# Kernel tuning notes

Hardware: AMD Instinct MI355X
Metric: run time of the kernel (lower is better)

## Reference

```python
import jax, jax.numpy as jnp
import numpy as np

# Coefficients expressing each of the 16 soft binary logic gates as
# c0 + ca*a + cb*b + cab*(a*b), in standard difflogic op order:
# 0:False 1:AND 2:a&~b 3:A 4:~a&b 5:B 6:XOR 7:OR 8:NOR 9:XNOR
# 10:~B 11:B=>A 12:~A 13:A=>B 14:NAND 15:True
GATE_COEF = jnp.array([
    [0, 0, 0, 0],
    [0, 0, 0, 1],
    [0, 1, 0, -1],
    [0, 1, 0, 0],
    [0, 0, 1, -1],
    [0, 0, 1, 0],
    [0, 1, 1, -2],
    [0, 1, 1, -1],
    [1, -1, -1, 1],
    [1, -1, -1, 2],
    [1, 0, -1, 0],
    [1, 0, -1, 1],
    [1, -1, 0, 0],
    [1, -1, 0, 1],
    [1, 0, 0, -1],
    [1, 0, 0, 0],
], dtype=jnp.float32)  # [16, 4]

INPUT_DIM = 8192
HIDDEN_DIMS = [16384, 16384, 16384, 16384]
OUTPUT_DIM = 1000
BATCH = 2048
TAU = 1.0
N_GATES = 16


def setup_inputs() -> dict:
    key = jax.random.key(0)
    kx, key = jax.random.split(key)
    inp = {"x": jax.random.uniform(kx, (BATCH, INPUT_DIM), dtype=jnp.float32)}
    dims = [INPUT_DIM] + HIDDEN_DIMS + [OUTPUT_DIM]
    for i in range(len(dims) - 1):
        in_d, out_d = dims[i], dims[i + 1]
        kw, ka, kb, key = jax.random.split(key, 4)
        inp[f"w{i}"] = jax.random.normal(kw, (out_d, N_GATES), dtype=jnp.float32)
        inp[f"ia{i}"] = jax.random.randint(ka, (out_d,), 0, in_d, dtype=jnp.int32)
        inp[f"ib{i}"] = jax.random.randint(kb, (out_d,), 0, in_d, dtype=jnp.int32)
    return inp


def _logic_layer(x, w, ia, ib):
    # gather the two inputs of every neuron: [batch, out_dim]
    a = x[:, ia]
    b = x[:, ib]
    p = jax.nn.softmax(w, axis=-1)              # [out_dim, 16]
    coef = p @ GATE_COEF                         # [out_dim, 4]
    # weighted mixture of all 16 gates, fused via bilinear form
    return coef[:, 0] + coef[:, 1] * a + coef[:, 2] * b + coef[:, 3] * (a * b)


def reference(x, w0, w1, w2, w3, w4, ia0, ia1, ia2, ia3, ia4, ib0, ib1, ib2, ib3, ib4):
    ws = [w0, w1, w2, w3, w4]
    ias = [ia0, ia1, ia2, ia3, ia4]
    ibs = [ib0, ib1, ib2, ib3, ib4]
    h = x
    for w, ia, ib in zip(ws, ias, ibs):
        h = _logic_layer(h, w, ia, ib)
    # GroupSum(output_dim, tau): split last dim into output_dim groups, sum, /tau
    batch = h.shape[0]
    group = h.shape[-1] // OUTPUT_DIM
    out = h.reshape(batch, OUTPUT_DIM, group).sum(-1) / TAU
    return out
```

## Files before the change

### kernel.cpp

```cpp
#include <hip/hip_runtime.h>


#define NBATCH 2048
#define IN_DIM 8192
#define HID 16384
#define OUT_DIM 1000
#define NTOT (4 * HID + OUT_DIM)

typedef __attribute__((ext_vector_type(4))) _Float16 half4;
typedef __attribute__((ext_vector_type(2))) _Float16 half2v;

__device__ __constant__ float GC_dev[64] = {
    0, 0, 0, 0,   0, 0, 0, 1,   0, 1, 0, -1,  0, 1, 0, 0,
    0, 0, 1, -1,  0, 0, 1, 0,   0, 1, 1, -2,  0, 1, 1, -1,
    1, -1, -1, 1, 1, -1, -1, 2, 1, 0, -1, 0,  1, 0, -1, 1,
    1, -1, 0, 0,  1, -1, 0, 1,  1, 0, 0, -1,  1, 0, 0, 0
};

struct PrepArgs {
    const float* w[5];
    const int* ia[5];
    const int* ib[5];
};

__global__ __launch_bounds__(256) void prep_kernel(
    PrepArgs args, half4* __restrict__ coefT, unsigned int* __restrict__ idxT) {
    int g = blockIdx.x * 256 + threadIdx.x;
    if (g >= NTOT) return;
    int l = (g < 4 * HID) ? (g >> 14) : 4;
    int j = g - l * HID;

    const float* wrow = args.w[l] + (size_t)j * 16;
    float v[16];
    const float4* w4 = (const float4*)wrow;
#pragma unroll
    for (int i = 0; i < 4; ++i) {
        float4 t = w4[i];
        v[4 * i + 0] = t.x; v[4 * i + 1] = t.y; v[4 * i + 2] = t.z; v[4 * i + 3] = t.w;
    }
    float m = v[0];
#pragma unroll
    for (int g2 = 1; g2 < 16; ++g2) m = fmaxf(m, v[g2]);
    float s = 0.f;
#pragma unroll
    for (int g2 = 0; g2 < 16; ++g2) { v[g2] = __expf(v[g2] - m); s += v[g2]; }
    float inv = 1.f / s;
    float c0 = 0.f, c1 = 0.f, c2 = 0.f, c3 = 0.f;
#pragma unroll
    for (int g2 = 0; g2 < 16; ++g2) {
        c0 += v[g2] * GC_dev[g2 * 4 + 0];
        c1 += v[g2] * GC_dev[g2 * 4 + 1];
        c2 += v[g2] * GC_dev[g2 * 4 + 2];
        c3 += v[g2] * GC_dev[g2 * 4 + 3];
    }
    half4 c;
    c[0] = (_Float16)(c0 * inv); c[1] = (_Float16)(c1 * inv);
    c[2] = (_Float16)(c2 * inv); c[3] = (_Float16)(c3 * inv);
    coefT[g] = c;
    idxT[g] = (unsigned int)args.ia[l][j] | ((unsigned int)args.ib[l][j] << 16);
}

__global__ __launch_bounds__(1024) void fused_kernel(
    const float* __restrict__ x, const half4* __restrict__ coefT,
    const unsigned int* __restrict__ idxT, float* __restrict__ out) {
    extern __shared__ half2v lds[];
    int bp = blockIdx.x;
    int t = threadIdx.x;
    int b0 = 2 * bp, b1 = 2 * bp + 1;

    const float4* xr0 = (const float4*)(x + (size_t)b0 * IN_DIM);
    const float4* xr1 = (const float4*)(x + (size_t)b1 * IN_DIM);
#pragma unroll
    for (int i = 0; i < 2; ++i) {
        int e = i * 1024 + t;
        float4 v0 = xr0[e];
        float4 v1 = xr1[e];
        half2v h0 = {(_Float16)v0.x, (_Float16)v1.x};
        half2v h1 = {(_Float16)v0.y, (_Float16)v1.y};
        half2v h2 = {(_Float16)v0.z, (_Float16)v1.z};
        half2v h3 = {(_Float16)v0.w, (_Float16)v1.w};
        lds[4 * e + 0] = h0;
        lds[4 * e + 1] = h1;
        lds[4 * e + 2] = h2;
        lds[4 * e + 3] = h3;
    }
    __syncthreads();

    int inW = 0, outW = HID;
    int tab = 0;
#pragma unroll
    for (int l = 0; l < 4; ++l) {
#pragma unroll 4
        for (int k = 0; k < HID / 1024; ++k) {
            int j = k * 1024 + t;
            unsigned int idx = idxT[tab + j];
            half4 c = coefT[tab + j];
            half2v ap = lds[inW + (idx & 0xFFFFu)];
            half2v bq = lds[inW + (idx >> 16)];
            float c0 = (float)c[0], c1 = (float)c[1];
            float c2 = (float)c[2], c3 = (float)c[3];
            float a0 = (float)ap[0], a1 = (float)ap[1];
            float q0 = (float)bq[0], q1 = (float)bq[1];
            float r0 = fmaf(c3, a0 * q0, fmaf(c2, q0, fmaf(c1, a0, c0)));
            float r1 = fmaf(c3, a1 * q1, fmaf(c2, q1, fmaf(c1, a1, c0)));
            half2v o = {(_Float16)r0, (_Float16)r1};
            lds[outW + j] = o;
        }
        tab += HID;
        int tmp = inW; inW = outW; outW = tmp;
        __syncthreads();
    }

    if (t < OUT_DIM) {
        unsigned int idx = idxT[tab + t];
        half4 c = coefT[tab + t];
        half2v ap = lds[idx & 0xFFFFu];
        half2v bq = lds[idx >> 16];
        float c0 = (float)c[0], c1 = (float)c[1];
        float c2 = (float)c[2], c3 = (float)c[3];
        float a0 = (float)ap[0], a1 = (float)ap[1];
        float q0 = (float)bq[0], q1 = (float)bq[1];
        out[(size_t)b0 * OUT_DIM + t] =
            fmaf(c3, a0 * q0, fmaf(c2, q0, fmaf(c1, a0, c0)));
        out[(size_t)b1 * OUT_DIM + t] =
            fmaf(c3, a1 * q1, fmaf(c2, q1, fmaf(c1, a1, c0)));
    }
}

extern "C" void kernel_launch(void* const* d_in, const int* in_sizes, int n_in,
                              void* d_out, int out_size, void* d_ws, size_t ws_size,
                              hipStream_t stream) {
    const float* x = (const float*)d_in[0];
    PrepArgs args;
    for (int i = 0; i < 5; ++i) {
        args.w[i]  = (const float*)d_in[1 + 3 * i];
        args.ia[i] = (const int*)d_in[2 + 3 * i];
        args.ib[i] = (const int*)d_in[3 + 3 * i];
    }

    char* ws = (char*)d_ws;
    half4* coefT = (half4*)ws;
    size_t coefBytes = ((size_t)NTOT * 8 + 255) & ~(size_t)255;
    unsigned int* idxT = (unsigned int*)(ws + coefBytes);

    prep_kernel<<<(NTOT + 255) / 256, 256, 0, stream>>>(args, coefT, idxT);
    fused_kernel<<<NBATCH / 2, 1024, 2 * HID * sizeof(half2v), stream>>>(
        x, coefT, idxT, (float*)d_out);
}
```

Baseline: 175.6 us.

## Process four batch rows per block with single in-place LDS buffer

Each block now handles four batch rows packed as half4 per LDS slot instead of two rows as half2, halving the block count. Coefficient and index loads are amortized over twice as many rows. Double buffering is replaced by keeping a layer's 16 results in registers, syncing, and then writing them back in place. LDS stays at 128KB, but register pressure rises from the 16 half4 results, and the extra barrier per layer may hurt at 1024 threads.

```diff
diff --git a/kernel.cpp b/kernel.cpp
--- a/kernel.cpp
+++ b/kernel.cpp
@@ -8,7 +8,6 @@
 #define NTOT (4 * HID + OUT_DIM)
 
 typedef __attribute__((ext_vector_type(4))) _Float16 half4;
-typedef __attribute__((ext_vector_type(2))) _Float16 half2v;
 
 __device__ __constant__ float GC_dev[64] = {
     0, 0, 0, 0,   0, 0, 0, 1,   0, 1, 0, -1,  0, 1, 0, 0,
@@ -63,67 +62,66 @@
 __global__ __launch_bounds__(1024) void fused_kernel(
     const float* __restrict__ x, const half4* __restrict__ coefT,
     const unsigned int* __restrict__ idxT, float* __restrict__ out) {
-    extern __shared__ half2v lds[];
+    extern __shared__ half4 lds[];
     int bp = blockIdx.x;
     int t = threadIdx.x;
-    int b0 = 2 * bp, b1 = 2 * bp + 1;
+    int r0 = 4 * bp;
 
-    const float4* xr0 = (const float4*)(x + (size_t)b0 * IN_DIM);
-    const float4* xr1 = (const float4*)(x + (size_t)b1 * IN_DIM);
+    const float* x0 = x + (size_t)r0 * IN_DIM;
 #pragma unroll
-    for (int i = 0; i < 2; ++i) {
-        int e = i * 1024 + t;
-        float4 v0 = xr0[e];
-        float4 v1 = xr1[e];
-        half2v h0 = {(_Float16)v0.x, (_Float16)v1.x};
-        half2v h1 = {(_Float16)v0.y, (_Float16)v1.y};
-        half2v h2 = {(_Float16)v0.z, (_Float16)v1.z};
-        half2v h3 = {(_Float16)v0.w, (_Float16)v1.w};
-        lds[4 * e + 0] = h0;
-        lds[4 * e + 1] = h1;
-        lds[4 * e + 2] = h2;
-        lds[4 * e + 3] = h3;
+    for (int i = 0; i < 8; ++i) {
+        int f = i * 1024 + t;
+        half4 h;
+        h[0] = (_Float16)x0[f];
+        h[1] = (_Float16)x0[IN_DIM + f];
+        h[2] = (_Float16)x0[2 * IN_DIM + f];
+        h[3] = (_Float16)x0[3 * IN_DIM + f];
+        lds[f] = h;
     }
     __syncthreads();
 
-    int inW = 0, outW = HID;
     int tab = 0;
+    for (int l = 0; l < 4; ++l) {
+        half4 res[16];
 #pragma unroll
-    for (int l = 0; l < 4; ++l) {
-#pragma unroll 4
-        for (int k = 0; k < HID / 1024; ++k) {
+        for (int k = 0; k < 16; ++k) {
             int j = k * 1024 + t;
             unsigned int idx = idxT[tab + j];
             half4 c = coefT[tab + j];
-            half2v ap = lds[inW + (idx & 0xFFFFu)];
-            half2v bq = lds[inW + (idx >> 16)];
+            half4 pa = lds[idx & 0xFFFFu];
+            half4 pb = lds[idx >> 16];
             float c0 = (float)c[0], c1 = (float)c[1];
             float c2 = (float)c[2], c3 = (float)c[3];
-            float a0 = (float)ap[0], a1 = (float)ap[1];
-            float q0 = (float)bq[0], q1 = (float)bq[1];
-            float r0 = fmaf(c3, a0 * q0, fmaf(c2, q0, fmaf(c1, a0, c0)));
-            float r1 = fmaf(c3, a1 * q1, fmaf(c2, q1, fmaf(c1, a1, c0)));
-            half2v o = {(_Float16)r0, (_Float16)r1};
-            lds[outW + j] = o;
+            half4 r;
+#pragma unroll
+            for (int i = 0; i < 4; ++i) {
+                float a = (float)pa[i];
+                float b = (float)pb[i];
+                r[i] = (_Float16)fmaf(fmaf(c3, b, c1), a, fmaf(c2, b, c0));
+            }
+            res[k] = r;
         }
+        __syncthreads();
+#pragma unroll
+        for (int k = 0; k < 16; ++k) lds[k * 1024 + t] = res[k];
         tab += HID;
-        int tmp = inW; inW = outW; outW = tmp;
         __syncthreads();
     }
 
     if (t < OUT_DIM) {
         unsigned int idx = idxT[tab + t];
         half4 c = coefT[tab + t];
-        half2v ap = lds[idx & 0xFFFFu];
-        half2v bq = lds[idx >> 16];
+        half4 pa = lds[idx & 0xFFFFu];
+        half4 pb = lds[idx >> 16];
         float c0 = (float)c[0], c1 = (float)c[1];
         float c2 = (float)c[2], c3 = (float)c[3];
-        float a0 = (float)ap[0], a1 = (float)ap[1];
-        float q0 = (float)bq[0], q1 = (float)bq[1];
-        out[(size_t)b0 * OUT_DIM + t] =
-            fmaf(c3, a0 * q0, fmaf(c2, q0, fmaf(c1, a0, c0)));
-        out[(size_t)b1 * OUT_DIM + t] =
-            fmaf(c3, a1 * q1, fmaf(c2, q1, fmaf(c1, a1, c0)));
+#pragma unroll
+        for (int i = 0; i < 4; ++i) {
+            float a = (float)pa[i];
+            float b = (float)pb[i];
+            out[(size_t)(r0 + i) * OUT_DIM + t] =
+                fmaf(fmaf(c3, b, c1), a, fmaf(c2, b, c0));
+        }
     }
 }
 
@@ -144,6 +142,6 @@
     unsigned int* idxT = (unsigned int*)(ws + coefBytes);
 
     prep_kernel<<<(NTOT + 255) / 256, 256, 0, stream>>>(args, coefT, idxT);
-    fused_kernel<<<NBATCH / 2, 1024, 2 * HID * sizeof(half2v), stream>>>(
+    fused_kernel<<<NBATCH / 4, 1024, HID * sizeof(half4), stream>>>(
         x, coefT, idxT, (float*)d_out);
 }
```

Result: slower. 194.3 us (+10.6%).

## Prune neurons not reachable from the outputs via backward liveness compaction

Applied to the files above, without the earlier changes.

A single-block build kernel walks the network backward from the 1000 output neurons, marks which hidden neurons are actually used, compacts them, and remaps gather indices. The fused kernel then evaluates only live neurons per layer, placing them at the ends of the LDS buffer so the buffers can alternate in place. This removes computation and table traffic for dead neurons, which random wiring makes a large fraction of the deeper layers. The cost is an extra serial single-block launch with many barriers, and the gate evaluation is also refactored into a nested-FMA form.

```diff
diff --git a/kernel.cpp b/kernel.cpp
--- a/kernel.cpp
+++ b/kernel.cpp
@@ -5,7 +5,8 @@
 #define IN_DIM 8192
 #define HID 16384
 #define OUT_DIM 1000
-#define NTOT (4 * HID + OUT_DIM)
+#define LDS_ENT 32768
+#define MARKV 0x7FFFFFFF
 
 typedef __attribute__((ext_vector_type(4))) _Float16 half4;
 typedef __attribute__((ext_vector_type(2))) _Float16 half2v;
@@ -17,26 +18,24 @@
     1, -1, 0, 0,  1, -1, 0, 1,  1, 0, 0, -1,  1, 0, 0, 0
 };
 
-struct PrepArgs {
+struct Tabs {
     const float* w[5];
     const int* ia[5];
     const int* ib[5];
 };
 
-__global__ __launch_bounds__(256) void prep_kernel(
-    PrepArgs args, half4* __restrict__ coefT, unsigned int* __restrict__ idxT) {
+__global__ __launch_bounds__(256) void coef_kernel(Tabs args, half4* __restrict__ coefFull) {
     int g = blockIdx.x * 256 + threadIdx.x;
-    if (g >= NTOT) return;
-    int l = (g < 4 * HID) ? (g >> 14) : 4;
-    int j = g - l * HID;
-
-    const float* wrow = args.w[l] + (size_t)j * 16;
+    int l = g >> 14;
+    int j = g & (HID - 1);
+    if (l == 4 && j >= OUT_DIM) return;
+
+    const float4* w4 = (const float4*)(args.w[l] + (size_t)j * 16);
     float v[16];
-    const float4* w4 = (const float4*)wrow;
 #pragma unroll
     for (int i = 0; i < 4; ++i) {
         float4 t = w4[i];
-        v[4 * i + 0] = t.x; v[4 * i + 1] = t.y; v[4 * i + 2] = t.z; v[4 * i + 3] = t.w;
+        v[4*i+0] = t.x; v[4*i+1] = t.y; v[4*i+2] = t.z; v[4*i+3] = t.w;
     }
     float m = v[0];
 #pragma unroll
@@ -48,25 +47,152 @@
     float c0 = 0.f, c1 = 0.f, c2 = 0.f, c3 = 0.f;
 #pragma unroll
     for (int g2 = 0; g2 < 16; ++g2) {
-        c0 += v[g2] * GC_dev[g2 * 4 + 0];
-        c1 += v[g2] * GC_dev[g2 * 4 + 1];
-        c2 += v[g2] * GC_dev[g2 * 4 + 2];
-        c3 += v[g2] * GC_dev[g2 * 4 + 3];
+        c0 += v[g2] * GC_dev[g2*4+0];
+        c1 += v[g2] * GC_dev[g2*4+1];
+        c2 += v[g2] * GC_dev[g2*4+2];
+        c3 += v[g2] * GC_dev[g2*4+3];
     }
     half4 c;
-    c[0] = (_Float16)(c0 * inv); c[1] = (_Float16)(c1 * inv);
-    c[2] = (_Float16)(c2 * inv); c[3] = (_Float16)(c3 * inv);
-    coefT[g] = c;
-    idxT[g] = (unsigned int)args.ia[l][j] | ((unsigned int)args.ib[l][j] << 16);
+    c[0] = (_Float16)(c0*inv); c[1] = (_Float16)(c1*inv);
+    c[2] = (_Float16)(c2*inv); c[3] = (_Float16)(c3*inv);
+    coefFull[g] = c;
+}
+
+__global__ __launch_bounds__(1024) void build_kernel(
+    Tabs args, const half4* __restrict__ coefFull,
+    unsigned int* __restrict__ tabIdx, half4* __restrict__ tabCoef,
+    int* __restrict__ header) {
+    __shared__ int mapA[HID];
+    __shared__ int mapB[HID];
+    __shared__ int cnt;
+    const int t = threadIdx.x;
+
+    for (int i = t; i < HID; i += 1024) mapA[i] = -1;
+    if (t == 0) cnt = 0;
+    __syncthreads();
+    if (t < OUT_DIM) { mapA[args.ia[4][t]] = MARKV; mapA[args.ib[4][t]] = MARKV; }
+    __syncthreads();
+    for (int i = t; i < HID; i += 1024)
+        if (mapA[i] == MARKV) mapA[i] = atomicAdd(&cnt, 1);
+    __syncthreads();
+    const int count3 = cnt;
+    if (t < OUT_DIM) {
+        unsigned a = (unsigned)(LDS_ENT - count3 + mapA[args.ia[4][t]]);
+        unsigned b = (unsigned)(LDS_ENT - count3 + mapA[args.ib[4][t]]);
+        tabIdx[4*HID + t] = a | (b << 16);
+        tabCoef[4*HID + t] = coefFull[4*HID + t];
+    }
+    __syncthreads();
+
+    for (int i = t; i < HID; i += 1024) mapB[i] = -1;
+    if (t == 0) cnt = 0;
+    __syncthreads();
+    for (int i = t; i < HID; i += 1024)
+        if (mapA[i] >= 0) { mapB[args.ia[3][i]] = MARKV; mapB[args.ib[3][i]] = MARKV; }
+    __syncthreads();
+    for (int i = t; i < HID; i += 1024)
+        if (mapB[i] == MARKV) mapB[i] = atomicAdd(&cnt, 1);
+    __syncthreads();
+    const int count2 = cnt;
+    for (int i = t; i < HID; i += 1024) {
+        int s = mapA[i];
+        if (s >= 0) {
+            unsigned a = 8192u + (unsigned)mapB[args.ia[3][i]];
+            unsigned b = 8192u + (unsigned)mapB[args.ib[3][i]];
+            tabIdx[3*HID + s] = a | (b << 16);
+            tabCoef[3*HID + s] = coefFull[3*HID + i];
+        }
+    }
+    __syncthreads();
+
+    for (int i = t; i < HID; i += 1024) mapA[i] = -1;
+    if (t == 0) cnt = 0;
+    __syncthreads();
+    for (int i = t; i < HID; i += 1024)
+        if (mapB[i] >= 0) { mapA[args.ia[2][i]] = MARKV; mapA[args.ib[2][i]] = MARKV; }
+    __syncthreads();
+    for (int i = t; i < HID; i += 1024)
+        if (mapA[i] == MARKV) mapA[i] = atomicAdd(&cnt, 1);
+    __syncthreads();
+    const int count1 = cnt;
+    {
+        unsigned base1 = (unsigned)(LDS_ENT - count1);
+        for (int i = t; i < HID; i += 1024) {
+            int s = mapB[i];
+            if (s >= 0) {
+                unsigned a = base1 + (unsigned)mapA[args.ia[2][i]];
+                unsigned b = base1 + (unsigned)mapA[args.ib[2][i]];
+                tabIdx[2*HID + s] = a | (b << 16);
+                tabCoef[2*HID + s] = coefFull[2*HID + i];
+            }
+        }
+    }
+    __syncthreads();
+
+    for (int i = t; i < HID; i += 1024) mapB[i] = -1;
+    if (t == 0) cnt = 0;
+    __syncthreads();
+    for (int i = t; i < HID; i += 1024)
+        if (mapA[i] >= 0) { mapB[args.ia[1][i]] = MARKV; mapB[args.ib[1][i]] = MARKV; }
+    __syncthreads();
+    for (int i = t; i < HID; i += 1024)
+        if (mapB[i] == MARKV) mapB[i] = atomicAdd(&cnt, 1);
+    __syncthreads();
+    const int count0 = cnt;
+    for (int i = t; i < HID; i += 1024) {
+        int s = mapA[i];
+        if (s >= 0) {
+            unsigned a = 8192u + (unsigned)mapB[args.ia[1][i]];
+            unsigned b = 8192u + (unsigned)mapB[args.ib[1][i]];
+            tabIdx[1*HID + s] = a | (b << 16);
+            tabCoef[1*HID + s] = coefFull[1*HID + i];
+        }
+    }
+    __syncthreads();
+
+    for (int i = t; i < HID; i += 1024) {
+        int s = mapB[i];
+        if (s >= 0) {
+            tabIdx[0*HID + s] =
+                (unsigned)args.ia[0][i] | ((unsigned)args.ib[0][i] << 16);
+            tabCoef[0*HID + s] = coefFull[0*HID + i];
+        }
+    }
+    if (t == 0) {
+        header[0] = count0; header[1] = count1;
+        header[2] = count2; header[3] = count3;
+    }
+}
+
+__device__ __forceinline__ void layer_pass(
+    half2v* lds, const unsigned* __restrict__ tIdx,
+    const half4* __restrict__ tCoef, int n, int wbase, int t) {
+    for (int j = t; j < n; j += 1024) {
+        unsigned idx = tIdx[j];
+        half4 c = tCoef[j];
+        half2v pa = lds[idx & 0xFFFFu];
+        half2v pb = lds[idx >> 16];
+        float c0 = (float)c[0], c1 = (float)c[1];
+        float c2 = (float)c[2], c3 = (float)c[3];
+        float a0 = (float)pa[0], a1 = (float)pa[1];
+        float q0 = (float)pb[0], q1 = (float)pb[1];
+        half2v o;
+        o[0] = (_Float16)fmaf(fmaf(c3, q0, c1), a0, fmaf(c2, q0, c0));
+        o[1] = (_Float16)fmaf(fmaf(c3, q1, c1), a1, fmaf(c2, q1, c0));
+        lds[wbase + j] = o;
+    }
+    __syncthreads();
 }
 
 __global__ __launch_bounds__(1024) void fused_kernel(
-    const float* __restrict__ x, const half4* __restrict__ coefT,
-    const unsigned int* __restrict__ idxT, float* __restrict__ out) {
+    const float* __restrict__ x, const unsigned* __restrict__ tabIdx,
+    const half4* __restrict__ tabCoef, const int* __restrict__ header,
+    float* __restrict__ out) {
     extern __shared__ half2v lds[];
     int bp = blockIdx.x;
     int t = threadIdx.x;
     int b0 = 2 * bp, b1 = 2 * bp + 1;
+    int n0 = header[0], n1 = header[1], n2 = header[2], n3 = header[3];
 
     const float4* xr0 = (const float4*)(x + (size_t)b0 * IN_DIM);
     const float4* xr1 = (const float4*)(x + (size_t)b1 * IN_DIM);
@@ -75,63 +201,38 @@
         int e = i * 1024 + t;
         float4 v0 = xr0[e];
         float4 v1 = xr1[e];
-        half2v h0 = {(_Float16)v0.x, (_Float16)v1.x};
-        half2v h1 = {(_Float16)v0.y, (_Float16)v1.y};
-        half2v h2 = {(_Float16)v0.z, (_Float16)v1.z};
-        half2v h3 = {(_Float16)v0.w, (_Float16)v1.w};
-        lds[4 * e + 0] = h0;
-        lds[4 * e + 1] = h1;
-        lds[4 * e + 2] = h2;
-        lds[4 * e + 3] = h3;
-    }
-    __syncthreads();
-
-    int inW = 0, outW = HID;
-    int tab = 0;
-#pragma unroll
-    for (int l = 0; l < 4; ++l) {
-#pragma unroll 4
-        for (int k = 0; k < HID / 1024; ++k) {
-            int j = k * 1024 + t;
-            unsigned int idx = idxT[tab + j];
-            half4 c = coefT[tab + j];
-            half2v ap = lds[inW + (idx & 0xFFFFu)];
-            half2v bq = lds[inW + (idx >> 16)];
-            float c0 = (float)c[0], c1 = (float)c[1];
-            float c2 = (float)c[2], c3 = (float)c[3];
-            float a0 = (float)ap[0], a1 = (float)ap[1];
-            float q0 = (float)bq[0], q1 = (float)bq[1];
-            float r0 = fmaf(c3, a0 * q0, fmaf(c2, q0, fmaf(c1, a0, c0)));
-            float r1 = fmaf(c3, a1 * q1, fmaf(c2, q1, fmaf(c1, a1, c0)));
-            half2v o = {(_Float16)r0, (_Float16)r1};
-            lds[outW + j] = o;
-        }
-        tab += HID;
-        int tmp = inW; inW = outW; outW = tmp;
-        __syncthreads();
-    }
+        half2v h0; h0[0] = (_Float16)v0.x; h0[1] = (_Float16)v1.x;
+        half2v h1; h1[0] = (_Float16)v0.y; h1[1] = (_Float16)v1.y;
+        half2v h2; h2[0] = (_Float16)v0.z; h2[1] = (_Float16)v1.z;
+        half2v h3; h3[0] = (_Float16)v0.w; h3[1] = (_Float16)v1.w;
+        lds[4*e+0] = h0; lds[4*e+1] = h1; lds[4*e+2] = h2; lds[4*e+3] = h3;
+    }
+    __syncthreads();
+
+    layer_pass(lds, tabIdx + 0*HID, tabCoef + 0*HID, n0, 8192,          t);
+    layer_pass(lds, tabIdx + 1*HID, tabCoef + 1*HID, n1, LDS_ENT - n1, t);
+    layer_pass(lds, tabIdx + 2*HID, tabCoef + 2*HID, n2, 8192,          t);
+    layer_pass(lds, tabIdx + 3*HID, tabCoef + 3*HID, n3, LDS_ENT - n3, t);
 
     if (t < OUT_DIM) {
-        unsigned int idx = idxT[tab + t];
-        half4 c = coefT[tab + t];
-        half2v ap = lds[idx & 0xFFFFu];
-        half2v bq = lds[idx >> 16];
+        unsigned idx = tabIdx[4*HID + t];
+        half4 c = tabCoef[4*HID + t];
+        half2v pa = lds[idx & 0xFFFFu];
+        half2v pb = lds[idx >> 16];
         float c0 = (float)c[0], c1 = (float)c[1];
         float c2 = (float)c[2], c3 = (float)c[3];
-        float a0 = (float)ap[0], a1 = (float)ap[1];
-        float q0 = (float)bq[0], q1 = (float)bq[1];
-        out[(size_t)b0 * OUT_DIM + t] =
-            fmaf(c3, a0 * q0, fmaf(c2, q0, fmaf(c1, a0, c0)));
-        out[(size_t)b1 * OUT_DIM + t] =
-            fmaf(c3, a1 * q1, fmaf(c2, q1, fmaf(c1, a1, c0)));
+        float a0 = (float)pa[0], a1 = (float)pa[1];
+        float q0 = (float)pb[0], q1 = (float)pb[1];
+        out[(size_t)b0 * OUT_DIM + t] = fmaf(fmaf(c3, q0, c1), a0, fmaf(c2, q0, c0));
+        out[(size_t)b1 * OUT_DIM + t] = fmaf(fmaf(c3, q1, c1), a1, fmaf(c2, q1, c0));
     }
 }
 
 extern "C" void kernel_launch(void* const* d_in, const int* in_sizes, int n_in,
                               void* d_out, int out_size, void* d_ws, size_t ws_size,
                               hipStream_t stream) {
+    Tabs args;
     const float* x = (const float*)d_in[0];
-    PrepArgs args;
     for (int i = 0; i < 5; ++i) {
         args.w[i]  = (const float*)d_in[1 + 3 * i];
         args.ia[i] = (const int*)d_in[2 + 3 * i];
@@ -139,11 +240,13 @@
     }
 
     char* ws = (char*)d_ws;
-    half4* coefT = (half4*)ws;
-    size_t coefBytes = ((size_t)NTOT * 8 + 255) & ~(size_t)255;
-    unsigned int* idxT = (unsigned int*)(ws + coefBytes);
-
-    prep_kernel<<<(NTOT + 255) / 256, 256, 0, stream>>>(args, coefT, idxT);
-    fused_kernel<<<NBATCH / 2, 1024, 2 * HID * sizeof(half2v), stream>>>(
-        x, coefT, idxT, (float*)d_out);
-}
+    half4* coefFull = (half4*)ws;
+    unsigned int* tabIdx = (unsigned int*)(ws + 655360);
+    half4* tabCoef = (half4*)(ws + 655360 + 327680);
+    int* header = (int*)(ws + 655360 + 327680 + 655360);
+
+    coef_kernel<<<5 * HID / 256, 256, 0, stream>>>(args, coefFull);
+    build_kernel<<<1, 1024, 0, stream>>>(args, coefFull, tabIdx, tabCoef, header);
+    fused_kernel<<<NBATCH / 2, 1024, LDS_ENT * sizeof(half2v), stream>>>(
+        x, tabIdx, tabCoef, header, (float*)d_out);
+}
```

After: 205.2 us. +16.8%, slower.
